# Performance work log

Hardware: AMD Instinct MI355X
Metric: run time of the kernel (lower is better)

## Reference

```python
import jax, jax.numpy as jnp
import numpy as np

Q = 4          # num_quantizers
K = 2048       # codebook_size
D = 256        # dim
B, N = 8, 8192 # batch, tokens (N % Q == 0)


def l2norm(t, eps=1e-12):
    return t / jnp.maximum(jnp.linalg.norm(t, axis=-1, keepdims=True), eps)


def setup_inputs() -> dict:
    key = jax.random.key(0)
    kx, ke = jax.random.split(key)
    x = jax.random.normal(kx, (B, N, D), dtype=jnp.float32)
    embed = jax.random.normal(ke, (Q, K, D), dtype=jnp.float32)
    return {"x": x, "embed": embed}


def reference(x, embed):
    b, n, d = x.shape
    q = embed.shape[0]
    m = n // q  # tokens per quantizer chunk
    # chunk along token axis (dim=1), as torch.chunk(x, Q, dim=1)
    xc = x.reshape(b, q, m, d).transpose(1, 0, 2, 3)  # [Q, B, M, D]

    def one_vq(xq, eq):
        # xq: [B, M, D], eq: [K, D]
        xn = l2norm(xq)
        en = l2norm(eq)
        dist = jnp.einsum('bmd,kd->bmk', xn, en)   # cosine similarity
        ind = jnp.argmax(dist, axis=-1)            # temp=0 gumbel -> argmax
        quant = eq[ind]                            # F.embedding with raw embed
        return quant, ind

    quant_c, ind_c = jax.vmap(one_vq)(xc, embed)   # [Q,B,M,D], [Q,B,M]
    quantized = quant_c.transpose(1, 0, 2, 3).reshape(b, n, d)
    encoding = ind_c.transpose(1, 0, 2).reshape(b, n)
    # eval mode: loss is sum of Q zero tensors of shape [1]
    vq_loss = jnp.zeros((1,), dtype=x.dtype)
    return quantized, encoding, vq_loss
```

## Files before the change

### kernel.cpp

```cpp
#include <hip/hip_runtime.h>
#include <math.h>

#define Bq 8
#define Nq 8192
#define Dq 256
#define Qq 4
#define Kq 2048
#define Mq (Nq / Qq)
#define TT (Bq * Nq)
#define QUANT_ELEMS ((size_t)TT * Dq)

#define CAP1Q 4096
#define THRESH 3e-4f
#define CAND_MAX 16

#define WS_CNT_OFF    0u
#define WS_LIST_OFF   1024u
#define WS_SX_OFF     66560u
#define WS_ENH_OFF    1377280u
#define WS_ENP_OFF    5571584u
#define WS_PART_OFF   13960192u

typedef __attribute__((ext_vector_type(8))) _Float16 f16x8;
typedef __attribute__((ext_vector_type(4))) _Float16 f16x4;
typedef __attribute__((ext_vector_type(4))) float    f32x4;

__device__ __forceinline__ void async_load16(const void* g, void* s) {
    __builtin_amdgcn_global_load_lds(
        (const __attribute__((address_space(1))) void*)g,
        (__attribute__((address_space(3))) void*)s, 16, 0, 0);
}

__device__ __forceinline__ float f32_div(float a, float b) {
    return (float)((double)a / (double)b);
}

__device__ __forceinline__ float np_norm_wave(const float* __restrict__ src, int ln) {
#pragma clang fp contract(off)
    float r = 0.0f;
    if (ln < 16) {
        const float* p = src + (ln >> 3) * 128 + (ln & 7);
        #pragma unroll
        for (int m = 0; m < 16; ++m) { float v = p[m * 8]; r = r + v * v; }
    }
    float t = r + __shfl_xor(r, 1, 64);
    t = t + __shfl_xor(t, 2, 64);
    t = t + __shfl_xor(t, 4, 64);
    float b0 = __shfl(t, 0, 64);
    float b1 = __shfl(t, 8, 64);
    float n2 = b0 + b1;
    return fmaxf((float)sqrt((double)n2), 1e-12f);
}

__global__ __launch_bounds__(256) void prep_kernel(const float* __restrict__ embed,
                                                   const float* __restrict__ x,
                                                   char* __restrict__ enh,
                                                   float* __restrict__ enp,
                                                   float* __restrict__ sxa,
                                                   int* __restrict__ cnt,
                                                   float* __restrict__ out) {
    if (blockIdx.x >= 2048) {
        const int tid = threadIdx.x;
        const int qd  = tid & 3;
        const int row = (blockIdx.x - 2048) * 64 + (tid >> 2);
        const float* xr = x + (size_t)row * Dq + qd * 8;
        float s2 = 0.f;
        #pragma unroll
        for (int ch = 0; ch < 8; ++ch) {
            float4 u = *(const float4*)(xr + ch * 32);
            float4 v = *(const float4*)(xr + ch * 32 + 4);
            s2 += u.x * u.x + u.y * u.y + u.z * u.z + u.w * u.w;
            s2 += v.x * v.x + v.y * v.y + v.z * v.z + v.w * v.w;
        }
        s2 += __shfl_xor(s2, 1, 64);
        s2 += __shfl_xor(s2, 2, 64);
        float sxv = 1.0f / fmaxf(sqrtf(s2), 1e-12f);
        if (qd == 0) sxa[row] = sxv;
        return;
    }

    if (blockIdx.x == 0) {
        if (threadIdx.x < 4) cnt[threadIdx.x] = 0;
        if (threadIdx.x == 0) out[QUANT_ELEMS + TT] = 0.0f;
    }

    int row = blockIdx.x * 4 + (threadIdx.x >> 6);
    int ln  = threadIdx.x & 63;
    const float* src = embed + (size_t)row * Dq;

    float4 v = *(const float4*)(src + ln * 4);
    float s = v.x * v.x + v.y * v.y + v.z * v.z + v.w * v.w;
    #pragma unroll
    for (int m = 1; m < 64; m <<= 1) s += __shfl_xor(s, m, 64);
    float sx = 1.0f / fmaxf(sqrtf(s), 1e-12f);
    int q = row >> 11, k = row & 2047, Tb = k >> 5, c = k & 31;
    int g = ln >> 1, h = ln & 1;
    f16x4 o;
    o[0] = (_Float16)(v.x * sx); o[1] = (_Float16)(v.y * sx);
    o[2] = (_Float16)(v.z * sx); o[3] = (_Float16)(v.w * sx);
    char* dst = enh + ((size_t)(q * 64 + Tb)) * 16384 + c * 512 + ((g ^ c) << 4) + h * 8;
    *(f16x4*)dst = o;

    float nm = np_norm_wave(src, ln);
    float* dstp = enp + (size_t)row * Dq;
    #pragma unroll
    for (int e = 0; e < 4; ++e) dstp[ln * 4 + e] = f32_div(src[ln * 4 + e], nm);
}

__global__ __launch_bounds__(256, 2) void gemm_kernel(const float* __restrict__ x,
                                                      const float* __restrict__ sxa,
                                                      const char* __restrict__ enh,
                                                      float4* __restrict__ part) {
    __shared__ __align__(16) char es[2][16384];

    const int tid = threadIdx.x;
    const int wv  = tid >> 6;
    const int ln  = tid & 63;
    const int qd  = ln >> 4;
    const int l15 = ln & 15;

    const int bid = blockIdx.x;
    const int h   = bid & 1;
    const int g   = bid >> 1;
    const int b   = g >> 5;
    const int rem = g & 31;
    const int q   = rem >> 3;
    const int m0  = (rem & 7) << 8;
    const int t0  = b * Nq + q * Mq + m0;
    const int t0w = t0 + wv * 64;

    f16x8 ah[4][8];
    #pragma unroll
    for (int mf = 0; mf < 4; ++mf) {
        const int tok = t0w + mf * 16 + l15;
        const float sxv = sxa[tok];
        const float* xr = x + (size_t)tok * Dq + qd * 8;
        #pragma unroll
        for (int ch = 0; ch < 8; ++ch) {
            float4 u = *(const float4*)(xr + ch * 32);
            float4 v = *(const float4*)(xr + ch * 32 + 4);
            f16x8 f;
            f[0] = (_Float16)(u.x * sxv); f[1] = (_Float16)(u.y * sxv);
            f[2] = (_Float16)(u.z * sxv); f[3] = (_Float16)(u.w * sxv);
            f[4] = (_Float16)(v.x * sxv); f[5] = (_Float16)(v.y * sxv);
            f[6] = (_Float16)(v.z * sxv); f[7] = (_Float16)(v.w * sxv);
            ah[mf][ch] = f;
        }
    }

    float b1[4][4], b2[4][4];
    int   ic[4][4];
    #pragma unroll
    for (int mf = 0; mf < 4; ++mf)
        #pragma unroll
        for (int r = 0; r < 4; ++r) { b1[mf][r] = -2.0f; b2[mf][r] = -2.0f; ic[mf][r] = 0; }

    const char* ebase = enh + ((size_t)(q * 64 + h * 32)) * 16384;

    #pragma unroll
    for (int i = 0; i < 4; ++i) {
        int off = i * 4096 + wv * 1024 + ln * 16;
        async_load16(ebase + off, es[0] + off);
    }
    __syncthreads();

    for (int T = 0; T < 32; ++T) {
        if (T + 1 < 32) {
            const char* src = ebase + (size_t)(T + 1) * 16384;
            #pragma unroll
            for (int i = 0; i < 4; ++i) {
                int off = i * 4096 + wv * 1024 + ln * 16;
                async_load16(src + off, es[(T + 1) & 1] + off);
            }
        }
        const char* esb = es[T & 1];

        #pragma unroll
        for (int s = 0; s < 2; ++s) {
            const int  c  = s * 16 + l15;
            const char* cb = esb + c * 512;
            f16x8 bfr[8];
            #pragma unroll
            for (int ch = 0; ch < 8; ++ch)
                bfr[ch] = *(const f16x8*)(cb + ((((ch << 2) | qd) ^ c) << 4));

            f32x4 a[4];
            #pragma unroll
            for (int mf = 0; mf < 4; ++mf) a[mf] = (f32x4){0.f, 0.f, 0.f, 0.f};
            #pragma unroll
            for (int ch = 0; ch < 8; ++ch) {
                #pragma unroll
                for (int mf = 0; mf < 4; ++mf)
                    a[mf] = __builtin_amdgcn_mfma_f32_16x16x32_f16(ah[mf][ch], bfr[ch], a[mf], 0, 0, 0);
            }

            const int cg = (h << 10) | (T << 5) | (s << 4) | l15;
            #pragma unroll
            for (int mf = 0; mf < 4; ++mf)
                #pragma unroll
                for (int r = 0; r < 4; ++r) {
                    float sv = a[mf][r];
                    bool  gt = sv > b1[mf][r];
                    b2[mf][r] = __builtin_amdgcn_fmed3f(sv, b1[mf][r], b2[mf][r]);
                    b1[mf][r] = fmaxf(b1[mf][r], sv);
                    ic[mf][r] = gt ? cg : ic[mf][r];
                }
        }
        __syncthreads();
    }

    float fb1[4][4], fb2[4][4];
    int   fic[4][4];
    #pragma unroll
    for (int mf = 0; mf < 4; ++mf)
        #pragma unroll
        for (int r = 0; r < 4; ++r) {
            float v1 = b1[mf][r], v2 = b2[mf][r]; int vi = ic[mf][r];
            #pragma unroll
            for (int m = 1; m < 16; m <<= 1) {
                float o1 = __shfl_xor(v1, m, 64);
                float o2 = __shfl_xor(v2, m, 64);
                int   oi = __shfl_xor(vi, m, 64);
                if (o1 > v1 || (o1 == v1 && oi < vi)) { v2 = fmaxf(v1, o2); v1 = o1; vi = oi; }
                else v2 = fmaxf(v2, o1);
            }
            fb1[mf][r] = v1; fb2[mf][r] = v2; fic[mf][r] = vi;
        }

    if (l15 == 0) {
        #pragma unroll
        for (int mf = 0; mf < 4; ++mf)
            #pragma unroll
            for (int r = 0; r < 4; ++r) {
                int t = t0w + mf * 16 + qd * 4 + r;
                float4 pv;
                pv.x = fb1[mf][r];
                pv.y = fb2[mf][r];
                pv.z = __int_as_float(fic[mf][r]);
                pv.w = 0.f;
                part[(size_t)h * TT + t] = pv;
            }
    }
}

__global__ __launch_bounds__(256) void merge_kernel(const float* __restrict__ embed,
                                                    const float4* __restrict__ part,
                                                    float* __restrict__ out,
                                                    int* __restrict__ cnt,
                                                    int* __restrict__ list) {
    const int wv = threadIdx.x >> 6, ln = threadIdx.x & 63;
    const int nw = gridDim.x * 4;

    for (int t = blockIdx.x * 4 + wv; t < TT; t += nw) {
        float4 pa = part[t];
        float4 pb = part[TT + t];
        float v1, v2; int vi;
        if (pb.x > pa.x) { v1 = pb.x; vi = __float_as_int(pb.z); v2 = fmaxf(pa.x, pb.y); }
        else             { v1 = pa.x; vi = __float_as_int(pa.z); v2 = fmaxf(pb.x, pa.y); }
        const int q = (t >> 11) & 3;

        if (ln == 0) {
            out[QUANT_ELEMS + (size_t)t] = (float)vi;
            if (v1 - v2 < THRESH) {
                int pos = atomicAdd(&cnt[q], 1);
                if (pos < CAP1Q) list[q * CAP1Q + pos] = t;
            }
        }
        const float* er = embed + ((size_t)(q * Kq + vi)) * Dq;
        float4 v = *(const float4*)(er + ln * 4);
        *(float4*)(out + (size_t)t * Dq + ln * 4) = v;
    }
}

__global__ __launch_bounds__(256) void cand_kernel(const float* __restrict__ x,
                                                   const float* __restrict__ sxa,
                                                   const char* __restrict__ enh,
                                                   const float* __restrict__ enp,
                                                   const float4* __restrict__ part,
                                                   const float* __restrict__ embed,
                                                   const int* __restrict__ cnt,
                                                   const int* __restrict__ list,
                                                   float* __restrict__ out) {
#pragma clang fp contract(off)
    __shared__ float xn[16][Dq];
    __shared__ int   stok[16];
    __shared__ float sv1[16];
    __shared__ int   scnt[16];
    __shared__ unsigned short scand[16][CAND_MAX];
    __shared__ float sc_s[256];
    __shared__ int   sc_c[256];
    __shared__ int   fbc[16];

    const int tid = threadIdx.x;
    const int wv  = tid >> 6;
    const int ln  = tid & 63;
    const int qd  = ln >> 4;
    const int l15 = ln & 15;

    int cq[4], nbq[4], total = 0;
    #pragma unroll
    for (int q = 0; q < 4; ++q) {
        int c = cnt[q]; if (c > CAP1Q) c = CAP1Q;
        cq[q] = c; nbq[q] = (c + 15) >> 4; total += nbq[q];
    }

    for (int j = blockIdx.x; j < total; j += gridDim.x) {
        int rem = j, q = 0;
        while (rem >= nbq[q]) { rem -= nbq[q]; ++q; }
        const int base = rem << 4;

        if (tid < 16) {
            int idx = base + tid;
            int tok = list[q * CAP1Q + (idx < cq[q] ? idx : base)];
            stok[tid] = tok;
            scnt[tid] = 0;
            sv1[tid]  = fmaxf(part[tok].x, part[TT + tok].x);
        }
        __syncthreads();

        f16x8 ah[8];
        {
            const int tok = stok[l15];
            const float sxv = sxa[tok];
            const float* xr = x + (size_t)tok * Dq + qd * 8;
            #pragma unroll
            for (int ch = 0; ch < 8; ++ch) {
                float4 u = *(const float4*)(xr + ch * 32);
                float4 v = *(const float4*)(xr + ch * 32 + 4);
                f16x8 f;
                f[0] = (_Float16)(u.x * sxv); f[1] = (_Float16)(u.y * sxv);
                f[2] = (_Float16)(u.z * sxv); f[3] = (_Float16)(u.w * sxv);
                f[4] = (_Float16)(v.x * sxv); f[5] = (_Float16)(v.y * sxv);
                f[6] = (_Float16)(v.z * sxv); f[7] = (_Float16)(v.w * sxv);
                ah[ch] = f;
            }
        }
        float thr[4];
        #pragma unroll
        for (int r = 0; r < 4; ++r) thr[r] = sv1[qd * 4 + r] - THRESH;

        const char* qbase = enh + ((size_t)(q * 64)) * 16384;
        for (int tt = 0; tt < 16; ++tt) {
            const int T = wv * 16 + tt;
            const char* tb = qbase + (size_t)T * 16384;
            #pragma unroll
            for (int s = 0; s < 2; ++s) {
                const int  c  = s * 16 + l15;
                const char* cb = tb + c * 512;
                f16x8 bfr[8];
                #pragma unroll
                for (int ch = 0; ch < 8; ++ch)
                    bfr[ch] = *(const f16x8*)(cb + ((((ch << 2) | qd) ^ c) << 4));

                f32x4 a = {0.f, 0.f, 0.f, 0.f};
                #pragma unroll
                for (int ch = 0; ch < 8; ++ch)
                    a = __builtin_amdgcn_mfma_f32_16x16x32_f16(ah[ch], bfr[ch], a, 0, 0, 0);

                const int cg = (T << 5) | (s << 4) | l15;
                #pragma unroll
                for (int r = 0; r < 4; ++r) {
                    if (a[r] >= thr[r]) {
                        int slot = qd * 4 + r;
                        int pos = atomicAdd(&scnt[slot], 1);
                        if (pos < CAND_MAX) scand[slot][pos] = (unsigned short)cg;
                    }
                }
            }
        }
        __syncthreads();

        for (int rr = 0; rr < 4; ++rr) {
            int i = wv * 4 + rr;
            const float* xr = x + (size_t)stok[i] * Dq;
            float nm = np_norm_wave(xr, ln);
            #pragma unroll
            for (int e = 0; e < 4; ++e)
                xn[i][ln * 4 + e] = f32_div(xr[ln * 4 + e], nm);
        }
        __syncthreads();

        {
            const int i = tid >> 4, sl = tid & 15;
            const int nc = scnt[i];
            float bs = -2.0f; int bc = 0x7fffffff;
            if (nc <= CAND_MAX && sl < nc) {
                int code = scand[i][sl];
                const float* er2 = enp + ((size_t)(q * Kq + code)) * Dq;
                float l0 = 0.f, l1 = 0.f, l2 = 0.f, l3 = 0.f;
                for (int d = 0; d < Dq; d += 4) {
                    float4 e = *(const float4*)(er2 + d);
                    float4 xv = *(const float4*)&xn[i][d];
                    l0 = l0 + xv.x * e.x; l1 = l1 + xv.y * e.y;
                    l2 = l2 + xv.z * e.z; l3 = l3 + xv.w * e.w;
                }
                bs = (l0 + l1) + (l2 + l3);
                bc = code;
            }
            sc_s[tid] = bs; sc_c[tid] = bc;
        }
        __syncthreads();
        if (tid < 16) {
            float bs = sc_s[tid * 16]; int bc = sc_c[tid * 16];
            #pragma unroll
            for (int sl = 1; sl < 16; ++sl) {
                float os = sc_s[tid * 16 + sl]; int oc = sc_c[tid * 16 + sl];
                if (os > bs || (os == bs && oc < bc)) { bs = os; bc = oc; }
            }
            fbc[tid] = bc;
        }
        __syncthreads();

        for (int i = 0; i < 16; ++i) {
            if (scnt[i] > CAND_MAX) {
                float bs = -2.0f; int bc = 0x7fffffff;
                for (int k = 0; k < 8; ++k) {
                    int code = k * 256 + tid;
                    const float* er2 = enp + ((size_t)(q * Kq + code)) * Dq;
                    float l0 = 0.f, l1 = 0.f, l2 = 0.f, l3 = 0.f;
                    for (int d = 0; d < Dq; d += 4) {
                        float4 e = *(const float4*)(er2 + d);
                        float4 xv = *(const float4*)&xn[i][d];
                        l0 = l0 + xv.x * e.x; l1 = l1 + xv.y * e.y;
                        l2 = l2 + xv.z * e.z; l3 = l3 + xv.w * e.w;
                    }
                    float sE = (l0 + l1) + (l2 + l3);
                    if (sE > bs || (sE == bs && code < bc)) { bs = sE; bc = code; }
                }
                sc_s[tid] = bs; sc_c[tid] = bc;
                __syncthreads();
                if (tid == 0) {
                    for (int t2 = 1; t2 < 256; ++t2) {
                        float os = sc_s[t2]; int oc = sc_c[t2];
                        if (os > bs || (os == bs && oc < bc)) { bs = os; bc = oc; }
                    }
                    fbc[i] = bc;
                }
                __syncthreads();
            }
        }

        for (int rr = 0; rr < 4; ++rr) {
            const int i = wv * 4 + rr;
            const int tok = stok[i];
            const int bc = fbc[i];
            if (ln == 0) out[QUANT_ELEMS + (size_t)tok] = (float)bc;
            const float* er = embed + ((size_t)(q * Kq + bc)) * Dq;
            float4 v = *(const float4*)(er + ln * 4);
            *(float4*)(out + (size_t)tok * Dq + ln * 4) = v;
        }
        __syncthreads();
    }
}

extern "C" void kernel_launch(void* const* d_in, const int* in_sizes, int n_in,
                              void* d_out, int out_size, void* d_ws, size_t ws_size,
                              hipStream_t stream) {
    const float* x     = (const float*)d_in[0];
    const float* embed = (const float*)d_in[1];
    float* out = (float*)d_out;
    char*  ws  = (char*)d_ws;
    int*    cnt    = (int*)(ws + WS_CNT_OFF);
    int*    list   = (int*)(ws + WS_LIST_OFF);
    float*  sxa    = (float*)(ws + WS_SX_OFF);
    char*   enh    = ws + WS_ENH_OFF;
    float*  enp    = (float*)(ws + WS_ENP_OFF);
    float4* part   = (float4*)(ws + WS_PART_OFF);

    prep_kernel<<<3072, 256, 0, stream>>>(embed, x, enh, enp, sxa, cnt, out);
    gemm_kernel<<<512, 256, 0, stream>>>(x, sxa, enh, part);
    merge_kernel<<<2048, 256, 0, stream>>>(embed, part, out, cnt, list);
    cand_kernel<<<1024, 256, 0, stream>>>(x, sxa, enh, enp, part, embed, cnt, list, out);
}
```

Baseline: 275.7 us.

## Triple-buffer codebook tiles in GEMM and skip writes for refined tokens in merge

The GEMM kernel moves from a double-buffered LDS codebook pipeline with two __syncthreads per tile to a three-stage ring buffer that prefetches two tiles ahead. It uses explicit vmcnt waits and a single s_barrier per iteration, so global loads overlap more of the MFMA work. The merge kernel stops writing the index and gathering the embedding row for tokens that were placed on the refinement candidate list, since cand_kernel rewrites those outputs anyway. In exchange, LDS use per block grows to 48KB, which could limit occupancy, and correctness now depends on the manual vmcnt counting.

```diff
diff --git a/kernel.cpp b/kernel.cpp
--- a/kernel.cpp
+++ b/kernel.cpp
@@ -111,7 +111,7 @@
                                                       const float* __restrict__ sxa,
                                                       const char* __restrict__ enh,
                                                       float4* __restrict__ part) {
-    __shared__ __align__(16) char es[2][16384];
+    __shared__ __align__(16) char es[3][16384];
 
     const int tid = threadIdx.x;
     const int wv  = tid >> 6;
@@ -148,6 +148,20 @@
         }
     }
 
+    const char* ebase = enh + ((size_t)(q * 64 + h * 32)) * 16384;
+    const int off0 = wv * 1024 + ln * 16;
+
+    __builtin_amdgcn_sched_barrier(0);
+    asm volatile("s_waitcnt vmcnt(0)");
+    __builtin_amdgcn_sched_barrier(0);
+    #pragma unroll
+    for (int i = 0; i < 4; ++i)
+        async_load16(ebase + i * 4096 + off0, es[0] + i * 4096 + off0);
+    #pragma unroll
+    for (int i = 0; i < 4; ++i)
+        async_load16(ebase + 16384 + i * 4096 + off0, es[1] + i * 4096 + off0);
+    __builtin_amdgcn_sched_barrier(0);
+
     float b1[4][4], b2[4][4];
     int   ic[4][4];
     #pragma unroll
@@ -155,25 +169,24 @@
         #pragma unroll
         for (int r = 0; r < 4; ++r) { b1[mf][r] = -2.0f; b2[mf][r] = -2.0f; ic[mf][r] = 0; }
 
-    const char* ebase = enh + ((size_t)(q * 64 + h * 32)) * 16384;
-
-    #pragma unroll
-    for (int i = 0; i < 4; ++i) {
-        int off = i * 4096 + wv * 1024 + ln * 16;
-        async_load16(ebase + off, es[0] + off);
-    }
-    __syncthreads();
-
+    int rb = 0;
     for (int T = 0; T < 32; ++T) {
-        if (T + 1 < 32) {
-            const char* src = ebase + (size_t)(T + 1) * 16384;
-            #pragma unroll
-            for (int i = 0; i < 4; ++i) {
-                int off = i * 4096 + wv * 1024 + ln * 16;
-                async_load16(src + off, es[(T + 1) & 1] + off);
-            }
-        }
-        const char* esb = es[T & 1];
+        if (T < 31) asm volatile("s_waitcnt vmcnt(4)");
+        else        asm volatile("s_waitcnt vmcnt(0)");
+        __builtin_amdgcn_sched_barrier(0);
+        __builtin_amdgcn_s_barrier();
+        __builtin_amdgcn_sched_barrier(0);
+
+        if (T + 2 < 32) {
+            int wb = rb + 2; if (wb >= 3) wb -= 3;
+            const char* src = ebase + (size_t)(T + 2) * 16384;
+            #pragma unroll
+            for (int i = 0; i < 4; ++i)
+                async_load16(src + i * 4096 + off0, es[wb] + i * 4096 + off0);
+        }
+        __builtin_amdgcn_sched_barrier(0);
+
+        const char* esb = es[rb];
 
         #pragma unroll
         for (int s = 0; s < 2; ++s) {
@@ -206,7 +219,7 @@
                     ic[mf][r] = gt ? cg : ic[mf][r];
                 }
         }
-        __syncthreads();
+        if (++rb == 3) rb = 0;
     }
 
     float fb1[4][4], fb2[4][4];
@@ -259,16 +272,20 @@
         else             { v1 = pa.x; vi = __float_as_int(pa.z); v2 = fmaxf(pb.x, pa.y); }
         const int q = (t >> 11) & 3;
 
+        int inlist = 0;
         if (ln == 0) {
-            out[QUANT_ELEMS + (size_t)t] = (float)vi;
             if (v1 - v2 < THRESH) {
                 int pos = atomicAdd(&cnt[q], 1);
-                if (pos < CAP1Q) list[q * CAP1Q + pos] = t;
-            }
-        }
-        const float* er = embed + ((size_t)(q * Kq + vi)) * Dq;
-        float4 v = *(const float4*)(er + ln * 4);
-        *(float4*)(out + (size_t)t * Dq + ln * 4) = v;
+                if (pos < CAP1Q) { list[q * CAP1Q + pos] = t; inlist = 1; }
+            }
+            if (!inlist) out[QUANT_ELEMS + (size_t)t] = (float)vi;
+        }
+        inlist = __shfl(inlist, 0, 64);
+        if (!inlist) {
+            const float* er = embed + ((size_t)(q * Kq + vi)) * Dq;
+            float4 v = *(const float4*)(er + ln * 4);
+            *(float4*)(out + (size_t)t * Dq + ln * 4) = v;
+        }
     }
 }
 
```

Result: no change. 279.4 us (+1.3%).

## Split codebook across four blocks per token tile and compact partial results

Applied to the files above, without the earlier changes.

The GEMM grid doubles from 512 to 1024 blocks, so each block scans a quarter of the codebook instead of half. This raises parallelism and shortens the per-block loop, but the x tile is reloaded twice as often. Partial top-2 results are stored as float2 plus a 16-bit index rather than float4, and merge combines four partials. Merge also skips writing the quantized row for tokens placed on the candidate list, since the candidate kernel rewrites them.

```diff
diff --git a/kernel.cpp b/kernel.cpp
--- a/kernel.cpp
+++ b/kernel.cpp
@@ -20,6 +20,7 @@
 #define WS_ENH_OFF    1377280u
 #define WS_ENP_OFF    5571584u
 #define WS_PART_OFF   13960192u
+#define WS_PIC_OFF    16057344u
 
 typedef __attribute__((ext_vector_type(8))) _Float16 f16x8;
 typedef __attribute__((ext_vector_type(4))) _Float16 f16x4;
@@ -110,7 +111,8 @@
 __global__ __launch_bounds__(256, 2) void gemm_kernel(const float* __restrict__ x,
                                                       const float* __restrict__ sxa,
                                                       const char* __restrict__ enh,
-                                                      float4* __restrict__ part) {
+                                                      float2* __restrict__ pb12,
+                                                      unsigned short* __restrict__ pic16) {
     __shared__ __align__(16) char es[2][16384];
 
     const int tid = threadIdx.x;
@@ -120,8 +122,8 @@
     const int l15 = ln & 15;
 
     const int bid = blockIdx.x;
-    const int h   = bid & 1;
-    const int g   = bid >> 1;
+    const int hh  = bid & 3;
+    const int g   = bid >> 2;
     const int b   = g >> 5;
     const int rem = g & 31;
     const int q   = rem >> 3;
@@ -155,7 +157,7 @@
         #pragma unroll
         for (int r = 0; r < 4; ++r) { b1[mf][r] = -2.0f; b2[mf][r] = -2.0f; ic[mf][r] = 0; }
 
-    const char* ebase = enh + ((size_t)(q * 64 + h * 32)) * 16384;
+    const char* ebase = enh + ((size_t)(q * 64 + hh * 16)) * 16384;
 
     #pragma unroll
     for (int i = 0; i < 4; ++i) {
@@ -164,8 +166,8 @@
     }
     __syncthreads();
 
-    for (int T = 0; T < 32; ++T) {
-        if (T + 1 < 32) {
+    for (int T = 0; T < 16; ++T) {
+        if (T + 1 < 16) {
             const char* src = ebase + (size_t)(T + 1) * 16384;
             #pragma unroll
             for (int i = 0; i < 4; ++i) {
@@ -194,7 +196,7 @@
                     a[mf] = __builtin_amdgcn_mfma_f32_16x16x32_f16(ah[mf][ch], bfr[ch], a[mf], 0, 0, 0);
             }
 
-            const int cg = (h << 10) | (T << 5) | (s << 4) | l15;
+            const int cg = (hh << 9) | (T << 5) | (s << 4) | l15;
             #pragma unroll
             for (int mf = 0; mf < 4; ++mf)
                 #pragma unroll
@@ -233,18 +235,16 @@
             #pragma unroll
             for (int r = 0; r < 4; ++r) {
                 int t = t0w + mf * 16 + qd * 4 + r;
-                float4 pv;
-                pv.x = fb1[mf][r];
-                pv.y = fb2[mf][r];
-                pv.z = __int_as_float(fic[mf][r]);
-                pv.w = 0.f;
-                part[(size_t)h * TT + t] = pv;
+                float2 pv; pv.x = fb1[mf][r]; pv.y = fb2[mf][r];
+                pb12 [(size_t)hh * TT + t] = pv;
+                pic16[(size_t)hh * TT + t] = (unsigned short)fic[mf][r];
             }
     }
 }
 
 __global__ __launch_bounds__(256) void merge_kernel(const float* __restrict__ embed,
-                                                    const float4* __restrict__ part,
+                                                    const float2* __restrict__ pb12,
+                                                    const unsigned short* __restrict__ pic16,
                                                     float* __restrict__ out,
                                                     int* __restrict__ cnt,
                                                     int* __restrict__ list) {
@@ -252,23 +252,32 @@
     const int nw = gridDim.x * 4;
 
     for (int t = blockIdx.x * 4 + wv; t < TT; t += nw) {
-        float4 pa = part[t];
-        float4 pb = part[TT + t];
-        float v1, v2; int vi;
-        if (pb.x > pa.x) { v1 = pb.x; vi = __float_as_int(pb.z); v2 = fmaxf(pa.x, pb.y); }
-        else             { v1 = pa.x; vi = __float_as_int(pa.z); v2 = fmaxf(pb.x, pa.y); }
+        float2 p0 = pb12[t];
+        float v1 = p0.x, v2 = p0.y;
+        int   vi = pic16[t];
+        #pragma unroll
+        for (int hh = 1; hh < 4; ++hh) {
+            float2 ph = pb12[(size_t)hh * TT + t];
+            int    ih = pic16[(size_t)hh * TT + t];
+            if (ph.x > v1) { v2 = fmaxf(v1, ph.y); v1 = ph.x; vi = ih; }
+            else           { v2 = fmaxf(v2, ph.x); }
+        }
         const int q = (t >> 11) & 3;
 
+        int inlist = 0;
         if (ln == 0) {
-            out[QUANT_ELEMS + (size_t)t] = (float)vi;
             if (v1 - v2 < THRESH) {
                 int pos = atomicAdd(&cnt[q], 1);
-                if (pos < CAP1Q) list[q * CAP1Q + pos] = t;
-            }
-        }
-        const float* er = embed + ((size_t)(q * Kq + vi)) * Dq;
-        float4 v = *(const float4*)(er + ln * 4);
-        *(float4*)(out + (size_t)t * Dq + ln * 4) = v;
+                if (pos < CAP1Q) { list[q * CAP1Q + pos] = t; inlist = 1; }
+            }
+            if (!inlist) out[QUANT_ELEMS + (size_t)t] = (float)vi;
+        }
+        inlist = __shfl(inlist, 0, 64);
+        if (!inlist) {
+            const float* er = embed + ((size_t)(q * Kq + vi)) * Dq;
+            float4 v = *(const float4*)(er + ln * 4);
+            *(float4*)(out + (size_t)t * Dq + ln * 4) = v;
+        }
     }
 }
 
@@ -276,7 +285,7 @@
                                                    const float* __restrict__ sxa,
                                                    const char* __restrict__ enh,
                                                    const float* __restrict__ enp,
-                                                   const float4* __restrict__ part,
+                                                   const float2* __restrict__ pb12,
                                                    const float* __restrict__ embed,
                                                    const int* __restrict__ cnt,
                                                    const int* __restrict__ list,
@@ -314,7 +323,9 @@
             int tok = list[q * CAP1Q + (idx < cq[q] ? idx : base)];
             stok[tid] = tok;
             scnt[tid] = 0;
-            sv1[tid]  = fmaxf(part[tok].x, part[TT + tok].x);
+            float m0 = fmaxf(pb12[tok].x,               pb12[(size_t)TT + tok].x);
+            float m1 = fmaxf(pb12[(size_t)2 * TT + tok].x, pb12[(size_t)3 * TT + tok].x);
+            sv1[tid]  = fmaxf(m0, m1);
         }
         __syncthreads();
 
@@ -460,15 +471,16 @@
     const float* embed = (const float*)d_in[1];
     float* out = (float*)d_out;
     char*  ws  = (char*)d_ws;
-    int*    cnt    = (int*)(ws + WS_CNT_OFF);
-    int*    list   = (int*)(ws + WS_LIST_OFF);
-    float*  sxa    = (float*)(ws + WS_SX_OFF);
-    char*   enh    = ws + WS_ENH_OFF;
-    float*  enp    = (float*)(ws + WS_ENP_OFF);
-    float4* part   = (float4*)(ws + WS_PART_OFF);
+    int*            cnt    = (int*)(ws + WS_CNT_OFF);
+    int*            list   = (int*)(ws + WS_LIST_OFF);
+    float*          sxa    = (float*)(ws + WS_SX_OFF);
+    char*           enh    = ws + WS_ENH_OFF;
+    float*          enp    = (float*)(ws + WS_ENP_OFF);
+    float2*         pb12   = (float2*)(ws + WS_PART_OFF);
+    unsigned short* pic16  = (unsigned short*)(ws + WS_PIC_OFF);
 
     prep_kernel<<<3072, 256, 0, stream>>>(embed, x, enh, enp, sxa, cnt, out);
-    gemm_kernel<<<512, 256, 0, stream>>>(x, sxa, enh, part);
-    merge_kernel<<<2048, 256, 0, stream>>>(embed, part, out, cnt, list);
-    cand_kernel<<<1024, 256, 0, stream>>>(x, sxa, enh, enp, part, embed, cnt, list, out);
-}
+    gemm_kernel<<<1024, 256, 0, stream>>>(x, sxa, enh, pb12, pic16);
+    merge_kernel<<<2048, 256, 0, stream>>>(embed, pb12, pic16, out, cnt, list);
+    cand_kernel<<<1024, 256, 0, stream>>>(x, sxa, enh, enp, pb12, embed, cnt, list, out);
+}
```

New measurement: 296.0 us. 1.07x slower.
